# Optimization experiments

Measured on AMD Instinct MI355X. Metric: run time of the kernel, lower is better.

Reference implementation:

```python
import jax, jax.numpy as jnp
from jax import lax
import numpy as np

WINDOW = 8
ENCOLEN = 128
HID = 128
INT_H = 128


def setup_inputs() -> dict:
    key = jax.random.key(0)
    ks = jax.random.split(key, 16)
    s = 0.05
    B, T = 512, 256
    return {
        "input_X": jax.random.normal(ks[0], (B, T, 7), jnp.float32),
        "W_ih": jax.random.normal(ks[1], (4 * HID, 5), jnp.float32) * s,
        "W_hh": jax.random.normal(ks[2], (4 * HID, HID), jnp.float32) * s,
        "b_ih": jax.random.normal(ks[3], (4 * HID,), jnp.float32) * s,
        "b_hh": jax.random.normal(ks[4], (4 * HID,), jnp.float32) * s,
        "fc1_w": jax.random.normal(ks[5], (HID, HID), jnp.float32) * s,
        "fc1_b": jax.random.normal(ks[6], (HID,), jnp.float32) * s,
        "fc2_w": jax.random.normal(ks[7], (1, HID), jnp.float32) * s,
        "fc2_b": jax.random.normal(ks[8], (1,), jnp.float32) * s,
        "int1_w": jax.random.normal(ks[9], (INT_H, 3), jnp.float32) * s,
        "int1_b": jax.random.normal(ks[10], (INT_H,), jnp.float32) * s,
        "int3_w": jax.random.normal(ks[11], (1, INT_H), jnp.float32) * s,
        "int3_b": jax.random.normal(ks[12], (1,), jnp.float32) * s,
        "scale_w": jax.random.normal(ks[13], (1, 1), jnp.float32) * s,
        "zone_w": jax.random.normal(ks[14], (1, 1), jnp.float32) * s,
    }


def _forward(input_X, W_ih, W_hh, b_ih, b_hh, fc1_w, fc1_b, fc2_w, fc2_b,
             int1_w, int1_b, int3_w, int3_b, scale_w, zone_w):
    B, T, _ = input_X.shape
    w = WINDOW
    T0 = input_X[:, :, 0:1]      # zone temperature
    Ext_X = input_X[:, :, 1:5]   # cols [1,2,3,4]
    Int_X = input_X[:, :, 3:6]   # cols [3,4,5]
    HVAC_X = input_X[:, :, 6:7]  # col [6]

    def lstm_chunk(h, c, xs):  # xs: [B, w, 5]
        def step(carry, x_t):
            h, c = carry
            g = x_t @ W_ih.T + b_ih + h @ W_hh.T + b_hh
            gi, gf, gg, go = jnp.split(g, 4, axis=-1)  # torch gate order i,f,g,o
            c = jax.nn.sigmoid(gf) * c + jax.nn.sigmoid(gi) * jnp.tanh(gg)
            h = jax.nn.sigmoid(go) * jnp.tanh(c)
            return (h, c), None
        (h, c), _ = lax.scan(step, (h, c), jnp.swapaxes(xs, 0, 1))
        return h, c  # final h == lstm_out[:, -1, :]

    def ext_module(h, c, xs):
        h, c = lstm_chunk(h, c, xs)
        o = jax.nn.relu(h @ fc1_w.T + fc1_b)
        return o @ fc2_w.T + fc2_b, h, c  # [B,1]

    # internal module is pointwise per timestep -> vectorize over all T
    # (note: FC2 in the torch module is defined but unused; faithful skip)
    int_all = jax.nn.sigmoid(
        jax.nn.relu(Int_X @ int1_w.T + int1_b) @ int3_w.T + int3_b
    ) @ scale_w.T  # [B,T,1]

    TOut = jnp.zeros((B, T, 1), input_X.dtype).at[:, :w].set(T0[:, :w])
    h = jnp.ones((B, HID), input_X.dtype)
    c = jnp.ones((B, HID), input_X.dtype)
    E = T0[:, w:w + 1, :]  # [B,1,1]

    def enc_step(carry, i):
        TOut, h, c, E = carry
        ratio = i.astype(input_X.dtype) / ENCOLEN
        TOut = lax.dynamic_update_slice(TOut, E, (0, i, 0))
        s = i - w + 1
        Tin = lax.dynamic_slice(T0, (0, s, 0), (B, w, 1))
        TOsl = lax.dynamic_slice(TOut, (0, s, 0), (B, w, 1))
        Exsl = lax.dynamic_slice(Ext_X, (0, s, 0), (B, w, 4))
        embed = jnp.concatenate([Tin * ratio + TOsl * (1.0 - ratio), Exsl], axis=2)
        ext, h, c = ext_module(h, c, embed)
        hv = lax.dynamic_slice(HVAC_X, (0, i, 0), (B, 1, 1))[:, 0]
        it = lax.dynamic_slice(int_all, (0, i, 0), (B, 1, 1))[:, 0]
        total = ext + hv + it  # [B,1]
        T0i = lax.dynamic_slice(T0, (0, i, 0), (B, 1, 1))
        E = ratio * T0i + (1.0 - ratio) * E + (total @ zone_w.T)[:, None, :]
        return (TOut, h, c, E), ext

    (TOut, h, c, E), ext_enc = lax.scan(enc_step, (TOut, h, c, E), jnp.arange(w, ENCOLEN))

    def dec_step(carry, i):
        TOut, h, c, E = carry
        TOut = lax.dynamic_update_slice(TOut, E, (0, i, 0))
        s = i - w + 1
        TOsl = lax.dynamic_slice(TOut, (0, s, 0), (B, w, 1))
        Exsl = lax.dynamic_slice(Ext_X, (0, s, 0), (B, w, 4))
        embed = jnp.concatenate([TOsl, Exsl], axis=2)
        ext, h, c = ext_module(h, c, embed)
        hv = lax.dynamic_slice(HVAC_X, (0, i, 0), (B, 1, 1))[:, 0]
        it = lax.dynamic_slice(int_all, (0, i, 0), (B, 1, 1))[:, 0]
        total = ext + hv + it
        E = (total @ zone_w.T)[:, None, :] + E
        return (TOut, h, c, E), ext

    (TOut, h, c, E), ext_dec = lax.scan(dec_step, (TOut, h, c, E), jnp.arange(ENCOLEN, T))

    Ext_list = jnp.zeros((B, T, 1), input_X.dtype)
    Ext_list = Ext_list.at[:, w:ENCOLEN].set(jnp.swapaxes(ext_enc, 0, 1))
    Ext_list = Ext_list.at[:, ENCOLEN:].set(jnp.swapaxes(ext_dec, 0, 1))
    Int_list = jnp.zeros((B, T, 1), input_X.dtype).at[:, w:].set(int_all[:, w:])
    HVAC_list = HVAC_X  # torch fills HVAC_list with HVAC_X at every step
    return TOut, HVAC_list, (Ext_list, Int_list)


def reference(input_X, W_ih, W_hh, b_ih, b_hh, fc1_w, fc1_b, fc2_w, fc2_b,
              int1_w, int1_b, int3_w, int3_b, scale_w, zone_w):
    return _forward(input_X, W_ih, W_hh, b_ih, b_hh, fc1_w, fc1_b, fc2_w, fc2_b,
                    int1_w, int1_b, int3_w, int3_b, scale_w, zone_w)
```

## Files before the change

### kernel.cpp

```cpp
#include <hip/hip_runtime.h>

#define BT   (512*256)
#define HB0b 128
#define HB1b 288
#define HLENb 448

using short8  = __attribute__((ext_vector_type(8))) short;
using floatx4 = __attribute__((ext_vector_type(4))) float;
using int4v   = __attribute__((ext_vector_type(4))) int;

__device__ inline unsigned short f2bf(float f){
  unsigned int u = __float_as_uint(f);
  u += 0x7FFFu + ((u >> 16) & 1u);
  return (unsigned short)(u >> 16);
}
__device__ inline float bf2f(unsigned short u){
  return __uint_as_float(((unsigned int)u) << 16);
}
__device__ inline float rcpf(float x){ return __builtin_amdgcn_rcpf(x); }

__global__ __launch_bounds__(512,1) void k_seq(
    const float* __restrict__ in,
    const float* __restrict__ Wih,  const float* __restrict__ Whh,
    const float* __restrict__ bih,  const float* __restrict__ bhh,
    const float* __restrict__ fc1w, const float* __restrict__ fc1b,
    const float* __restrict__ fc2w, const float* __restrict__ fc2b,
    const float* __restrict__ i1w,  const float* __restrict__ i1b,
    const float* __restrict__ i3w,  const float* __restrict__ i3b,
    const float* __restrict__ scw,  const float* __restrict__ zonew,
    float* __restrict__ out)
{
  __shared__ __align__(16) signed char hbuf[2][HLENb];
  __shared__ __align__(16) unsigned short xg[8192];
  __shared__ __align__(8)  unsigned short toutl[512];
  __shared__ __align__(8)  unsigned short extl[512];
  __shared__ __align__(16) unsigned short exl[2048];
  __shared__ float t0l[512];
  __shared__ float hvitl[512];
  __shared__ float parts[16];

  const int tid = threadIdx.x;
  const int wv  = tid >> 6;
  const int ln  = tid & 63;
  const int l15 = ln & 15;
  const int quad= ln >> 4;
  const int bb  = blockIdx.x;

  {
    int b=tid>>8, tt=tid&255;
    const float* row = in + (2*bb+b)*1792 + tt*7;
    t0l[tid] = row[0];
    exl[tid*4+0]=f2bf(row[1]); exl[tid*4+1]=f2bf(row[2]);
    exl[tid*4+2]=f2bf(row[3]); exl[tid*4+3]=f2bf(row[4]);
  }
  for(int p=tid; p<2*HLENb; p+=512) ((signed char*)hbuf)[p]=0;
  if(tid<16) toutl[(tid>>3)*256+(tid&7)] = f2bf(in[(2*bb+(tid>>3))*1792+(tid&7)*7]);
  float* lw4 = (float*)&xg[0];
  float* l3  = lw4 + 512;
  if(tid<128){
    lw4[tid*4+0]=i1w[tid*3+0]; lw4[tid*4+1]=i1w[tid*3+1];
    lw4[tid*4+2]=i1w[tid*3+2]; lw4[tid*4+3]=i1b[tid];
    l3[tid]=i3w[tid];
  }
  __syncthreads();
  if(tid<256) hbuf[0][((tid>>7)? HB1b:HB0b) + (tid&127)] = 127;

  {
    const float b30=i3b[0], sc0=scw[0];
    int b=tid>>8, t=tid&255;
    const float* row = in + (2*bb+b)*1792 + t*7;
    float x0=row[3],x1=row[4],x2=row[5], acc=0.f;
    #pragma unroll 8
    for(int j=0;j<128;j++){
      float r=fmaxf(lw4[j*4]*x0+lw4[j*4+1]*x1+lw4[j*4+2]*x2+lw4[j*4+3],0.f);
      acc += r*l3[j];
    }
    float v = rcpf(1.f+__expf(-(acc+b30)))*sc0;
    float itv = (t<8)?0.f:v;
    int gb = 2*bb+b;
    hvitl[tid] = row[6] + itv;
    out[3*BT+gb*256+t]=itv;
    out[BT+gb*256+t]=row[6];
    if(t<8){ out[gb*256+t]=row[0]; out[2*BT+gb*256+t]=0.f; }
  }

  int4v wq[4][2];
  float dq[4];
  short8 xfr[4];
  float  bsum[4];
  #pragma unroll
  for(int g=0;g<4;g++){
    int n = 128*g + 16*wv + l15;
    bsum[g] = bih[n]+bhh[n];
    const float* wr = Whh + n*128;
    float mx = 1e-20f;
    for(int j=0;j<128;j++) mx = fmaxf(mx, fabsf(wr[j]));
    float qs = 127.f/mx;
    dq[g] = mx * (1.f/16129.f);
    #pragma unroll
    for(int c=0;c<2;c++){
      int4v v4;
      #pragma unroll
      for(int d=0;d<4;d++){
        int pk=0;
        #pragma unroll
        for(int bq=0;bq<4;bq++){
          int kk = c*64 + quad*16 + d*4 + bq;
          int q = __float2int_rn(wr[kk]*qs);
          pk |= (q & 255) << (8*bq);
        }
        v4[d]=pk;
      }
      wq[g][c]=v4;
    }
    short8 f;
    #pragma unroll
    for(int j=0;j<8;j++){ int kk=quad*8+j; f[j]=(short)f2bf(kk<5?Wih[n*5+kk]:0.f); }
    xfr[g]=f;
  }
  int4v fq[2]; float dqf;
  {
    int n2 = 16*wv + l15;
    const float* fr = fc1w + n2*128;
    float mx = 1e-20f;
    for(int j=0;j<128;j++) mx = fmaxf(mx, fabsf(fr[j]));
    float qs = 127.f/mx;
    dqf = mx * (1.f/16129.f);
    #pragma unroll
    for(int c=0;c<2;c++){
      int4v v4;
      #pragma unroll
      for(int d=0;d<4;d++){
        int pk=0;
        #pragma unroll
        for(int bq=0;bq<4;bq++){
          int kk = c*64 + quad*16 + d*4 + bq;
          int q = __float2int_rn(fr[kk]*qs);
          pk |= (q & 255) << (8*bq);
        }
        v4[d]=pk;
      }
      fq[c]=v4;
    }
  }

  const int  u     = 16*wv + l15;
  const int  bm    = quad & 1;
  const int  arow  = ((l15&3)==0) ? (((l15>>2)&1)? HB1b : HB0b) : 0;
  const int  aoff  = arow + quad*16;
  const int  xbase = bm*512 + u;
  const int  hwoff = (bm? HB1b:HB0b) + u;
  const float fb    = fc1b[u];
  const float fcw_u = fc2w[u];
  const float fc2b0 = fc2b[0];
  const float zwv   = zonew[0];
  const floatx4 ZV  = {0.f,0.f,0.f,0.f};
  const int4v   ZI  = {0,0,0,0};
  const short8  Z8  = 0;
  float E0 = in[(2*bb)*1792 + 56];
  float E1 = in[(2*bb+1)*1792 + 56];
  float c0 = 1.f;
  __syncthreads();

  #pragma unroll 1
  for(int i=8;i<256;i++){
    if(i>8){
      float ext0 = parts[0]+parts[2]+parts[4]+parts[6]
                 + parts[8]+parts[10]+parts[12]+parts[14] + fc2b0;
      float ext1 = parts[1]+parts[3]+parts[5]+parts[7]
                 + parts[9]+parts[11]+parts[13]+parts[15] + fc2b0;
      int ip = i-1;
      float tot0 = ext0 + hvitl[ip];
      float tot1 = ext1 + hvitl[256+ip];
      if(ip<128){
        float ratio=(float)ip*0.0078125f;
        E0 = ratio*t0l[ip]     + (1.f-ratio)*E0 + tot0*zwv;
        E1 = ratio*t0l[256+ip] + (1.f-ratio)*E1 + tot1*zwv;
      } else {
        E0 += tot0*zwv;
        E1 += tot1*zwv;
      }
      if(tid==0){ extl[ip]=f2bf(ext0); extl[256+ip]=f2bf(ext1); }
    }
    if(tid==0){ toutl[i]=f2bf(E0); toutl[256+i]=f2bf(E1); }
    {
      short8 ea = Z8;
      if(quad==0){
        int bE=l15>>3, kk=l15&7, p=i-7+kk;
        float tos = (p==i) ? (bE? E1:E0) : bf2f(toutl[bE*256+p]);
        float tmix;
        if(i<128){
          float ratio=(float)i*0.0078125f;
          tmix = t0l[bE*256+p]*ratio + tos*(1.f-ratio);
        } else tmix = tos;
        ea[0]=(short)f2bf(tmix);
        ea[1]=(short)exl[(bE*256+p)*4+0]; ea[2]=(short)exl[(bE*256+p)*4+1];
        ea[3]=(short)exl[(bE*256+p)*4+2]; ea[4]=(short)exl[(bE*256+p)*4+3];
      }
      #pragma unroll
      for(int g=0;g<4;g++){
        floatx4 z=__builtin_amdgcn_mfma_f32_16x16x32_bf16(ea, xfr[g], ZV,0,0,0);
        #pragma unroll
        for(int r=0;r<4;r++){
          int m=4*quad+r;
          xg[(m&7)*1024 + (m>>3)*512 + 128*g + u] = f2bf(z[r]+bsum[g]);
        }
      }
    }
    __syncthreads();

    #pragma unroll
    for(int k=0;k<8;k++){
      float xv0=bf2f(xg[k*1024+xbase    ]);
      float xv1=bf2f(xg[k*1024+xbase+128]);
      float xv2=bf2f(xg[k*1024+xbase+256]);
      float xv3=bf2f(xg[k*1024+xbase+384]);
      const signed char* hb = &hbuf[k&1][0];
      int4v a0 = *(const int4v*)(hb + aoff);
      int4v a1 = *(const int4v*)(hb + aoff + 64);
      int4v acc[4];
      #pragma unroll
      for(int g=0;g<4;g++){
        int4v z = __builtin_amdgcn_mfma_i32_16x16x64_i8(a0, wq[g][0], ZI,0,0,0);
        z = __builtin_amdgcn_mfma_i32_16x16x64_i8(a1, wq[g][1], z,0,0,0);
        acc[g]=z;
      }
      float gi=(float)acc[0][0]*dq[0]+xv0;
      float gf=(float)acc[1][0]*dq[1]+xv1;
      float gg=(float)acc[2][0]*dq[2]+xv2;
      float go=(float)acc[3][0]*dq[3]+xv3;
      float ef =__expf(-gf);
      float egi=__expf(-gi);
      float egg=__expf(-2.f*gg);
      float sf = rcpf(1.f+ef);
      float itn=(1.f-egg)*rcpf((1.f+egi)*(1.f+egg));
      c0 = sf*c0 + itn;
      float ego=__expf(-go);
      float ec =__expf(-2.f*c0);
      float hv2=(1.f-ec)*rcpf((1.f+ego)*(1.f+ec));
      int q = __float2int_rn(hv2*127.f);
      hbuf[(k+1)&1][hwoff] = (signed char)q;
      __syncthreads();
    }

    {
      const signed char* hb = &hbuf[0][0];
      int4v a0 = *(const int4v*)(hb + aoff);
      int4v a1 = *(const int4v*)(hb + aoff + 64);
      int4v z = __builtin_amdgcn_mfma_i32_16x16x64_i8(a0, fq[0], ZI,0,0,0);
      z = __builtin_amdgcn_mfma_i32_16x16x64_i8(a1, fq[1], z,0,0,0);
      float fv = (float)z[0]*dqf + fb;
      float pv = fmaxf(fv,0.f)*fcw_u;
      float v0 = (quad==0) ? pv : 0.f;
      float v1 = (quad==1) ? pv : 0.f;
      #pragma unroll
      for(int off=32; off; off>>=1){
        v0 += __shfl_xor(v0, off, 64);
        v1 += __shfl_xor(v1, off, 64);
      }
      if(ln==0){ parts[wv*2]=v0; parts[wv*2+1]=v1; }
    }
    __syncthreads();
  }

  if(tid==0){
    float ext0 = parts[0]+parts[2]+parts[4]+parts[6]
               + parts[8]+parts[10]+parts[12]+parts[14] + fc2b0;
    float ext1 = parts[1]+parts[3]+parts[5]+parts[7]
               + parts[9]+parts[11]+parts[13]+parts[15] + fc2b0;
    extl[255]=f2bf(ext0); extl[511]=f2bf(ext1);
  }
  __syncthreads();

  for(int p=tid; p<496; p+=512){
    int b = (p>=248) ? 1 : 0;
    int i2 = p - b*248 + 8;
    int gb = 2*bb + b;
    out[gb*256+i2]      = bf2f(toutl[b*256+i2]);
    out[2*BT+gb*256+i2] = bf2f(extl[b*256+i2]);
  }
}

extern "C" void kernel_launch(void* const* d_in, const int* in_sizes, int n_in,
                              void* d_out, int out_size, void* d_ws, size_t ws_size,
                              hipStream_t stream)
{
  const float* in   = (const float*)d_in[0];
  const float* Wih  = (const float*)d_in[1];
  const float* Whh  = (const float*)d_in[2];
  const float* bih  = (const float*)d_in[3];
  const float* bhh  = (const float*)d_in[4];
  const float* fc1w = (const float*)d_in[5];
  const float* fc1b = (const float*)d_in[6];
  const float* fc2w = (const float*)d_in[7];
  const float* fc2b = (const float*)d_in[8];
  const float* i1w  = (const float*)d_in[9];
  const float* i1b  = (const float*)d_in[10];
  const float* i3w  = (const float*)d_in[11];
  const float* i3b  = (const float*)d_in[12];
  const float* scw  = (const float*)d_in[13];
  const float* zw   = (const float*)d_in[14];
  float* out = (float*)d_out;

  k_seq<<<dim3(256), dim3(512), 0, stream>>>(in, Wih, Whh, bih, bhh,
                                             fc1w, fc1b, fc2w, fc2b,
                                             i1w, i1b, i3w, i3b, scw, zw, out);
}
```

Before: 1.082 ms.

## Route input-gate projections through ds_bpermute and fold log2e into weights

Input-projection MFMA results are no longer staged in a shared bf16 buffer. They now go straight to the consuming lanes via ds_bpermute held in registers, which removes one block-wide barrier per timestep and keeps those values in fp32. Log2(e) is folded into the biases, Wih and the dequant scales so the gates use exp2 directly. The fc reduction shuffles only within 16-lane groups, parts are read as vector loads, and the hbuf offsets change. The cost is higher register pressure from the 32 per-thread xv values.

After: 969.3 us. -10.4%, faster.

```diff
diff --git a/kernel.cpp b/kernel.cpp
--- a/kernel.cpp
+++ b/kernel.cpp
@@ -1,13 +1,15 @@
 #include <hip/hip_runtime.h>
 
 #define BT   (512*256)
-#define HB0b 128
-#define HB1b 288
+#define HB0b 192
+#define HB1b 320
 #define HLENb 448
+#define LOG2E 1.44269504088896f
 
 using short8  = __attribute__((ext_vector_type(8))) short;
 using floatx4 = __attribute__((ext_vector_type(4))) float;
 using int4v   = __attribute__((ext_vector_type(4))) int;
+using ushort4v= __attribute__((ext_vector_type(4))) unsigned short;
 
 __device__ inline unsigned short f2bf(float f){
   unsigned int u = __float_as_uint(f);
@@ -18,6 +20,7 @@
   return __uint_as_float(((unsigned int)u) << 16);
 }
 __device__ inline float rcpf(float x){ return __builtin_amdgcn_rcpf(x); }
+__device__ inline float ex2(float x){ return __builtin_amdgcn_exp2f(x); }
 
 __global__ __launch_bounds__(512,1) void k_seq(
     const float* __restrict__ in,
@@ -31,13 +34,13 @@
     float* __restrict__ out)
 {
   __shared__ __align__(16) signed char hbuf[2][HLENb];
-  __shared__ __align__(16) unsigned short xg[8192];
+  __shared__ __align__(16) float scratch[640];
   __shared__ __align__(8)  unsigned short toutl[512];
   __shared__ __align__(8)  unsigned short extl[512];
   __shared__ __align__(16) unsigned short exl[2048];
   __shared__ float t0l[512];
   __shared__ float hvitl[512];
-  __shared__ float parts[16];
+  __shared__ __align__(16) float parts[16];
 
   const int tid = threadIdx.x;
   const int wv  = tid >> 6;
@@ -55,8 +58,8 @@
   }
   for(int p=tid; p<2*HLENb; p+=512) ((signed char*)hbuf)[p]=0;
   if(tid<16) toutl[(tid>>3)*256+(tid&7)] = f2bf(in[(2*bb+(tid>>3))*1792+(tid&7)*7]);
-  float* lw4 = (float*)&xg[0];
-  float* l3  = lw4 + 512;
+  float* lw4 = scratch;
+  float* l3  = scratch + 512;
   if(tid<128){
     lw4[tid*4+0]=i1w[tid*3+0]; lw4[tid*4+1]=i1w[tid*3+1];
     lw4[tid*4+2]=i1w[tid*3+2]; lw4[tid*4+3]=i1b[tid];
@@ -91,12 +94,12 @@
   #pragma unroll
   for(int g=0;g<4;g++){
     int n = 128*g + 16*wv + l15;
-    bsum[g] = bih[n]+bhh[n];
+    bsum[g] = (bih[n]+bhh[n])*LOG2E;
     const float* wr = Whh + n*128;
     float mx = 1e-20f;
     for(int j=0;j<128;j++) mx = fmaxf(mx, fabsf(wr[j]));
     float qs = 127.f/mx;
-    dq[g] = mx * (1.f/16129.f);
+    dq[g] = mx * (LOG2E/16129.f);
     #pragma unroll
     for(int c=0;c<2;c++){
       int4v v4;
@@ -115,7 +118,7 @@
     }
     short8 f;
     #pragma unroll
-    for(int j=0;j<8;j++){ int kk=quad*8+j; f[j]=(short)f2bf(kk<5?Wih[n*5+kk]:0.f); }
+    for(int j=0;j<8;j++){ int kk=quad*8+j; f[j]=(short)f2bf(kk<5?Wih[n*5+kk]*LOG2E:0.f); }
     xfr[g]=f;
   }
   int4v fq[2]; float dqf;
@@ -148,8 +151,9 @@
   const int  bm    = quad & 1;
   const int  arow  = ((l15&3)==0) ? (((l15>>2)&1)? HB1b : HB0b) : 0;
   const int  aoff  = arow + quad*16;
-  const int  xbase = bm*512 + u;
   const int  hwoff = (bm? HB1b:HB0b) + u;
+  const int  bpa0  = ((quad&1)<<7) | (l15<<2);
+  const int  bpa1  = bpa0 + 64;
   const float fb    = fc1b[u];
   const float fcw_u = fc2w[u];
   const float fc2b0 = fc2b[0];
@@ -165,10 +169,12 @@
   #pragma unroll 1
   for(int i=8;i<256;i++){
     if(i>8){
-      float ext0 = parts[0]+parts[2]+parts[4]+parts[6]
-                 + parts[8]+parts[10]+parts[12]+parts[14] + fc2b0;
-      float ext1 = parts[1]+parts[3]+parts[5]+parts[7]
-                 + parts[9]+parts[11]+parts[13]+parts[15] + fc2b0;
+      floatx4 pa=*(const floatx4*)&parts[0];
+      floatx4 pb=*(const floatx4*)&parts[4];
+      floatx4 pc=*(const floatx4*)&parts[8];
+      floatx4 pd=*(const floatx4*)&parts[12];
+      float ext0=((pa[0]+pa[1])+(pa[2]+pa[3]))+((pb[0]+pb[1])+(pb[2]+pb[3]))+fc2b0;
+      float ext1=((pc[0]+pc[1])+(pc[2]+pc[3]))+((pd[0]+pd[1])+(pd[2]+pd[3]))+fc2b0;
       int ip = i-1;
       float tot0 = ext0 + hvitl[ip];
       float tot1 = ext1 + hvitl[256+ip];
@@ -183,6 +189,7 @@
       if(tid==0){ extl[ip]=f2bf(ext0); extl[256+ip]=f2bf(ext1); }
     }
     if(tid==0){ toutl[i]=f2bf(E0); toutl[256+i]=f2bf(E1); }
+    float xv[8][4];
     {
       short8 ea = Z8;
       if(quad==0){
@@ -194,27 +201,24 @@
           tmix = t0l[bE*256+p]*ratio + tos*(1.f-ratio);
         } else tmix = tos;
         ea[0]=(short)f2bf(tmix);
-        ea[1]=(short)exl[(bE*256+p)*4+0]; ea[2]=(short)exl[(bE*256+p)*4+1];
-        ea[3]=(short)exl[(bE*256+p)*4+2]; ea[4]=(short)exl[(bE*256+p)*4+3];
+        ushort4v e4 = *(const ushort4v*)&exl[(bE*256+p)*4];
+        ea[1]=(short)e4[0]; ea[2]=(short)e4[1];
+        ea[3]=(short)e4[2]; ea[4]=(short)e4[3];
       }
       #pragma unroll
       for(int g=0;g<4;g++){
         floatx4 z=__builtin_amdgcn_mfma_f32_16x16x32_bf16(ea, xfr[g], ZV,0,0,0);
         #pragma unroll
         for(int r=0;r<4;r++){
-          int m=4*quad+r;
-          xg[(m&7)*1024 + (m>>3)*512 + 128*g + u] = f2bf(z[r]+bsum[g]);
+          int zi = __float_as_int(z[r]+bsum[g]);
+          xv[r][g]   = __int_as_float(__builtin_amdgcn_ds_bpermute(bpa0, zi));
+          xv[r+4][g] = __int_as_float(__builtin_amdgcn_ds_bpermute(bpa1, zi));
         }
       }
     }
-    __syncthreads();
 
     #pragma unroll
     for(int k=0;k<8;k++){
-      float xv0=bf2f(xg[k*1024+xbase    ]);
-      float xv1=bf2f(xg[k*1024+xbase+128]);
-      float xv2=bf2f(xg[k*1024+xbase+256]);
-      float xv3=bf2f(xg[k*1024+xbase+384]);
       const signed char* hb = &hbuf[k&1][0];
       int4v a0 = *(const int4v*)(hb + aoff);
       int4v a1 = *(const int4v*)(hb + aoff + 64);
@@ -225,18 +229,18 @@
         z = __builtin_amdgcn_mfma_i32_16x16x64_i8(a1, wq[g][1], z,0,0,0);
         acc[g]=z;
       }
-      float gi=(float)acc[0][0]*dq[0]+xv0;
-      float gf=(float)acc[1][0]*dq[1]+xv1;
-      float gg=(float)acc[2][0]*dq[2]+xv2;
-      float go=(float)acc[3][0]*dq[3]+xv3;
-      float ef =__expf(-gf);
-      float egi=__expf(-gi);
-      float egg=__expf(-2.f*gg);
+      float gi=fmaf((float)acc[0][0],dq[0],xv[k][0]);
+      float gf=fmaf((float)acc[1][0],dq[1],xv[k][1]);
+      float gg=fmaf((float)acc[2][0],dq[2],xv[k][2]);
+      float go=fmaf((float)acc[3][0],dq[3],xv[k][3]);
+      float ef =ex2(-gf);
+      float egi=ex2(-gi);
+      float egg=ex2(-2.f*gg);
       float sf = rcpf(1.f+ef);
       float itn=(1.f-egg)*rcpf((1.f+egi)*(1.f+egg));
       c0 = sf*c0 + itn;
-      float ego=__expf(-go);
-      float ec =__expf(-2.f*c0);
+      float ego=ex2(-go);
+      float ec =ex2(-2.8853900818f*c0);
       float hv2=(1.f-ec)*rcpf((1.f+ego)*(1.f+ec));
       int q = __float2int_rn(hv2*127.f);
       hbuf[(k+1)&1][hwoff] = (signed char)q;
@@ -251,23 +255,21 @@
       z = __builtin_amdgcn_mfma_i32_16x16x64_i8(a1, fq[1], z,0,0,0);
       float fv = (float)z[0]*dqf + fb;
       float pv = fmaxf(fv,0.f)*fcw_u;
-      float v0 = (quad==0) ? pv : 0.f;
-      float v1 = (quad==1) ? pv : 0.f;
-      #pragma unroll
-      for(int off=32; off; off>>=1){
-        v0 += __shfl_xor(v0, off, 64);
-        v1 += __shfl_xor(v1, off, 64);
-      }
-      if(ln==0){ parts[wv*2]=v0; parts[wv*2+1]=v1; }
+      pv += __shfl_xor(pv, 1, 64);
+      pv += __shfl_xor(pv, 2, 64);
+      pv += __shfl_xor(pv, 4, 64);
+      pv += __shfl_xor(pv, 8, 64);
+      if(ln==0)       parts[wv]   = pv;
+      else if(ln==16) parts[8+wv] = pv;
     }
     __syncthreads();
   }
 
   if(tid==0){
-    float ext0 = parts[0]+parts[2]+parts[4]+parts[6]
-               + parts[8]+parts[10]+parts[12]+parts[14] + fc2b0;
-    float ext1 = parts[1]+parts[3]+parts[5]+parts[7]
-               + parts[9]+parts[11]+parts[13]+parts[15] + fc2b0;
+    float ext0 = ((parts[0]+parts[1])+(parts[2]+parts[3]))
+               + ((parts[4]+parts[5])+(parts[6]+parts[7])) + fc2b0;
+    float ext1 = ((parts[8]+parts[9])+(parts[10]+parts[11]))
+               + ((parts[12]+parts[13])+(parts[14]+parts[15])) + fc2b0;
     extl[255]=f2bf(ext0); extl[511]=f2bf(ext1);
   }
   __syncthreads();
```
